# Kernel optimization log

Measured on AMD Instinct MI355X. Metric: run time of the kernel, lower is better.

## Reference

```python
import jax, jax.numpy as jnp
import numpy as np
from jax import lax

B, T, N = 512, 512, 64  # batch, max_seq_len, num_tags


def setup_inputs() -> dict:
    key = jax.random.key(0)
    k1, k2, k3, k4 = jax.random.split(key, 4)
    inputs = jax.random.normal(k1, (B, T, N), dtype=jnp.float32)
    transition_params = jax.random.normal(k2, (N, N), dtype=jnp.float32)
    tag_indices = jax.random.randint(k3, (B, T), 0, N, dtype=jnp.int32)
    sequence_lengths = jax.random.randint(k4, (B,), 0, T, dtype=jnp.int32)
    return {
        "inputs": inputs,
        "transition_params": transition_params,
        "tag_indices": tag_indices,
        "sequence_lengths": sequence_lengths,
    }


def _crf_log_norm(inputs, transition_params, sequence_lengths):
    # inputs: [B, T, N]
    first = inputs[:, 0, :]                       # alpha after first token, [B, N]
    rest = jnp.transpose(inputs[:, 1:, :], (1, 0, 2))  # [T-1, B, N]

    def step(alpha, emit):
        # alpha: [B, N] -> broadcast-add transitions [N, N], logsumexp over prev tag
        new = emit + jax.nn.logsumexp(alpha[:, :, None] + transition_params[None], axis=1)
        return new, new

    _, alphas = lax.scan(step, first, rest)       # [T-1, B, N]
    all_alphas = jnp.concatenate([first[None], alphas], axis=0)  # [T, B, N]
    all_alphas = jnp.transpose(all_alphas, (1, 0, 2))            # [B, T, N]
    last_index = jnp.maximum(0, sequence_lengths - 1)            # [B]
    alpha_last = jnp.take_along_axis(all_alphas, last_index[:, None, None], axis=1)[:, 0, :]
    return jax.nn.logsumexp(alpha_last, axis=1)   # [B]


def _crf_sequence_score(inputs, tag_indices, sequence_lengths, transition_params):
    mask = (jnp.arange(T)[None, :] < sequence_lengths[:, None]).astype(inputs.dtype)  # [B, T]
    # unary: gather emission score of the gold tag at each position
    unary = jnp.take_along_axis(inputs, tag_indices[:, :, None], axis=2)[:, :, 0]      # [B, T]
    unary_scores = jnp.sum(unary * mask, axis=1)
    # binary: transition scores between consecutive gold tags
    binary = transition_params[tag_indices[:, :-1], tag_indices[:, 1:]]                # [B, T-1]
    binary_scores = jnp.sum(binary * mask[:, 1:], axis=1)
    return unary_scores + binary_scores


def reference(inputs, transition_params, tag_indices, sequence_lengths):
    tag_indices = tag_indices.astype(jnp.int32)
    sequence_lengths = sequence_lengths.astype(jnp.int32)
    sequence_scores = _crf_sequence_score(inputs, tag_indices, sequence_lengths, transition_params)
    log_norm = _crf_log_norm(inputs, transition_params, sequence_lengths)
    log_likelihood = sequence_scores - log_norm   # [B]
    return (log_likelihood, transition_params)
```

## Files before the change

kernel.cpp:

```cpp
#include <hip/hip_runtime.h>

#define BB 512
#define TT 512
#define NN 64

__device__ __forceinline__ float readlane_f(float v, int lane) {
    return __int_as_float(__builtin_amdgcn_readlane(__float_as_int(v), lane));
}


#define S2(x) #x
#define S1(x) S2(x)

#define FMAC_DPP(ACC, QB, EV, R) \
    asm("v_fmac_f32_dpp %0, %1, %2 row_ror:" S1(R) " row_mask:0xf bank_mask:0xf" \
        : "+v"(ACC) : "v"(QB), "v"(EV));
#define MUL_DPP(DST, QB, EV, R) \
    asm("v_mul_f32_dpp %0, %1, %2 row_ror:" S1(R) " row_mask:0xf bank_mask:0xf" \
        : "=v"(DST) : "v"(QB), "v"(EV));

#define BLK_FIRST(QB, C0, C1, C2, C3) \
    a0 = QB * C0.x; \
    MUL_DPP(a1, QB, C0.y, 1)  MUL_DPP(a2, QB, C0.z, 2)  MUL_DPP(a3, QB, C0.w, 3) \
    FMAC_DPP(a0, QB, C1.x, 4)  FMAC_DPP(a1, QB, C1.y, 5) \
    FMAC_DPP(a2, QB, C1.z, 6)  FMAC_DPP(a3, QB, C1.w, 7) \
    FMAC_DPP(a0, QB, C2.x, 8)  FMAC_DPP(a1, QB, C2.y, 9) \
    FMAC_DPP(a2, QB, C2.z, 10) FMAC_DPP(a3, QB, C2.w, 11) \
    FMAC_DPP(a0, QB, C3.x, 12) FMAC_DPP(a1, QB, C3.y, 13) \
    FMAC_DPP(a2, QB, C3.z, 14) FMAC_DPP(a3, QB, C3.w, 15)

#define BLK(QB, C0, C1, C2, C3) \
    a0 = fmaf(QB, C0.x, a0); \
    FMAC_DPP(a1, QB, C0.y, 1)  FMAC_DPP(a2, QB, C0.z, 2)  FMAC_DPP(a3, QB, C0.w, 3) \
    FMAC_DPP(a0, QB, C1.x, 4)  FMAC_DPP(a1, QB, C1.y, 5) \
    FMAC_DPP(a2, QB, C1.z, 6)  FMAC_DPP(a3, QB, C1.w, 7) \
    FMAC_DPP(a0, QB, C2.x, 8)  FMAC_DPP(a1, QB, C2.y, 9) \
    FMAC_DPP(a2, QB, C2.z, 10) FMAC_DPP(a3, QB, C2.w, 11) \
    FMAC_DPP(a0, QB, C3.x, 12) FMAC_DPP(a1, QB, C3.y, 13) \
    FMAC_DPP(a2, QB, C3.z, 14) FMAC_DPP(a3, QB, C3.w, 15)

#define STEP(tc_, EM, RESC) { \
    asm("s_nop 1" : "+v"(q));    \
    const int qi = __float_as_int(q); \
    const float q1 = __int_as_float(__builtin_amdgcn_ds_bpermute(a16, qi)); \
    const float q2 = __int_as_float(__builtin_amdgcn_ds_bpermute(a32, qi)); \
    const float q3 = __int_as_float(__builtin_amdgcn_ds_bpermute(a48, qi)); \
    float a0, a1, a2, a3; \
    BLK_FIRST(q, D00, D01, D02, D03) \
    BLK(q1, D10, D11, D12, D13) \
    BLK(q2, D20, D21, D22, D23) \
    BLK(q3, D30, D31, D32, D33) \
    const float s = (a0 + a1) + (a2 + a3); \
    float qn; \
    if (RESC) { \
        const int sb = __float_as_int(readlane_f(s, 0)); \
        const int kb = ((sb >> 23) & 255) - 127; \
        const float sf = __int_as_float((127 - kb) << 23);   \
        qn = (s * (EM)) * sf; \
        if ((tc_) <= last) kcum += kb; \
    } else { \
        qn = s * (EM); \
    } \
    q = ((tc_) <= last) ? qn : q; \
}

__global__ __launch_bounds__(64, 1) void crf_kernel(
    const float* __restrict__ inputs,
    const float* __restrict__ trans,
    const int*   __restrict__ tags,
    const int*   __restrict__ lens,
    float*       __restrict__ out)
{
    const int b = blockIdx.x;
    const int j = threadIdx.x;

    if (b < 64) out[BB + b * 64 + j] = trans[b * 64 + j];

    const int L    = lens[b];
    const int last = (L - 1) > 0 ? (L - 1) : 0;

    const float* inb  = inputs + (size_t)b * TT * NN;
    const int*   tagb = tags + (size_t)b * TT;

    float sc = 0.f;
    #pragma unroll
    for (int k = 0; k < 8; ++k) {
        const int t  = k * 64 + j;
        const int tg = tagb[t];
        if (t < L) sc += inb[t * NN + tg];
        if (t + 1 < L) sc += trans[tg * NN + tagb[t + 1]];
    }
    #pragma unroll
    for (int x = 32; x >= 1; x >>= 1) sc += __shfl_xor(sc, x, 64);

    const int pr  = __builtin_amdgcn_update_dpp(0, j, 0x121 ,
                                                0xf, 0xf, false);
    const int r0p = __builtin_amdgcn_readlane(pr, 0);
    const int dhw = (r0p == 1) ? 1 : -1;

    float4 D00, D01, D02, D03, D10, D11, D12, D13;
    float4 D20, D21, D22, D23, D30, D31, D32, D33;
#define LDD(DST, B, R) { \
    const int rr = (j + dhw * (R)) & 15; \
    const int ii = (((j & 48) | rr) + 16 * (B)) & 63; \
    DST = __expf(trans[ii * NN + j]); }
#define LDD4(V, B, R0) LDD(V.x, B, R0) LDD(V.y, B, (R0)+1) \
                       LDD(V.z, B, (R0)+2) LDD(V.w, B, (R0)+3)
    LDD4(D00, 0, 0) LDD4(D01, 0, 4) LDD4(D02, 0, 8) LDD4(D03, 0, 12)
    LDD4(D10, 1, 0) LDD4(D11, 1, 4) LDD4(D12, 1, 8) LDD4(D13, 1, 12)
    LDD4(D20, 2, 0) LDD4(D21, 2, 4) LDD4(D22, 2, 8) LDD4(D23, 2, 12)
    LDD4(D30, 3, 0) LDD4(D31, 3, 4) LDD4(D32, 3, 8) LDD4(D33, 3, 12)
#undef LDD4
#undef LDD

    const int a16 = ((j + 16) & 63) * 4;
    const int a32 = ((j + 32) & 63) * 4;
    const int a48 = ((j + 48) & 63) * 4;

    const float alpha0 = inb[j];
    const float m0 = readlane_f(alpha0, 0);
    float q = __expf(alpha0 - m0);
    int kcum = 0;

    float4 fA0, fA1, fB0, fB1;

#define LD(vec, comp, tt) { const int tc_ = (tt) <= last ? (tt) : last; \
                            vec.comp = inb[tc_ * NN + j]; }
#define LOAD8(v0, v1, base) \
    LD(v0, x, (base) + 0) LD(v0, y, (base) + 1) LD(v0, z, (base) + 2) LD(v0, w, (base) + 3) \
    LD(v1, x, (base) + 4) LD(v1, y, (base) + 5) LD(v1, z, (base) + 6) LD(v1, w, (base) + 7)
#define EXP8(v0, v1) \
    v0.x = __expf(v0.x); v0.y = __expf(v0.y); v0.z = __expf(v0.z); v0.w = __expf(v0.w); \
    v1.x = __expf(v1.x); v1.y = __expf(v1.y); v1.z = __expf(v1.z); v1.w = __expf(v1.w);

    LOAD8(fA0, fA1, 1)
    EXP8(fA0, fA1)

    for (int t0 = 1; t0 <= last; t0 += 16) {
        LOAD8(fB0, fB1, t0 + 8)
        STEP(t0 + 0, fA0.x, 0) STEP(t0 + 1, fA0.y, 0)
        STEP(t0 + 2, fA0.z, 0) STEP(t0 + 3, fA0.w, 1)
        STEP(t0 + 4, fA1.x, 0) STEP(t0 + 5, fA1.y, 0)
        STEP(t0 + 6, fA1.z, 0) STEP(t0 + 7, fA1.w, 1)
        EXP8(fB0, fB1)
        LOAD8(fA0, fA1, t0 + 16)
        STEP(t0 + 8,  fB0.x, 0) STEP(t0 + 9,  fB0.y, 0)
        STEP(t0 + 10, fB0.z, 0) STEP(t0 + 11, fB0.w, 1)
        STEP(t0 + 12, fB1.x, 0) STEP(t0 + 13, fB1.y, 0)
        STEP(t0 + 14, fB1.z, 0) STEP(t0 + 15, fB1.w, 1)
        EXP8(fA0, fA1)
    }
#undef EXP8
#undef LOAD8
#undef LD

    float qs = q;
    #pragma unroll
    for (int x = 32; x >= 1; x >>= 1) qs += __shfl_xor(qs, x, 64);
    if (j == 0) {
        const double C = (double)m0 + (double)kcum * 0.6931471805599453;
        out[b] = sc - (float)((double)__logf(qs) + C);
    }
}

extern "C" void kernel_launch(void* const* d_in, const int* in_sizes, int n_in,
                              void* d_out, int out_size, void* d_ws, size_t ws_size,
                              hipStream_t stream) {
    const float* inputs = (const float*)d_in[0];
    const float* trans  = (const float*)d_in[1];
    const int*   tags   = (const int*)d_in[2];
    const int*   lens   = (const int*)d_in[3];
    float*       out    = (float*)d_out;

    crf_kernel<<<dim3(BB), dim3(64), 0, stream>>>(inputs, trans, tags, lens, out);
}
```

Measured before the change: 202.7 us.

## Stream exp-transition coefficients from LDS each step instead of holding in registers

The 64 precomputed exp(transition) values per lane are stored in shared memory in an XOR-swizzled layout, and each recurrence step re-reads them with ds_read_b128 into registers, issued after the step together with the three bpermutes. Hand-written asm with explicit lgkmcnt waits and sched barriers controls the ordering. The aim is to cut register pressure or free the scheduler, and to overlap the LDS reads with the cross-lane bpermute latency. In exchange, every one of the roughly 512 serial steps now issues 16 extra LDS loads and waits on all of them before its FMACs can run.

Result: slower. 226.2 us (+11.6%).

```diff
diff --git a/kernel.cpp b/kernel.cpp
--- a/kernel.cpp
+++ b/kernel.cpp
@@ -1,4 +1,5 @@
 #include <hip/hip_runtime.h>
+#include <stdint.h>
 
 #define BB 512
 #define TT 512
@@ -13,11 +14,17 @@
 #define S1(x) S2(x)
 
 #define FMAC_DPP(ACC, QB, EV, R) \
-    asm("v_fmac_f32_dpp %0, %1, %2 row_ror:" S1(R) " row_mask:0xf bank_mask:0xf" \
+    asm volatile("v_fmac_f32_dpp %0, %1, %2 row_ror:" S1(R) " row_mask:0xf bank_mask:0xf" \
         : "+v"(ACC) : "v"(QB), "v"(EV));
 #define MUL_DPP(DST, QB, EV, R) \
-    asm("v_mul_f32_dpp %0, %1, %2 row_ror:" S1(R) " row_mask:0xf bank_mask:0xf" \
+    asm volatile("v_mul_f32_dpp %0, %1, %2 row_ror:" S1(R) " row_mask:0xf bank_mask:0xf" \
         : "=v"(DST) : "v"(QB), "v"(EV));
+#define RD1(Cv, AD) \
+    asm volatile("ds_read_b128 %0, %1" : "=v"(Cv) : "v"(AD));
+#define BPERM(DST, AD, SRC) \
+    asm volatile("ds_bpermute_b32 %0, %1, %2" : "=v"(DST) : "v"(AD), "v"(SRC));
+#define WAITLG0 { asm volatile("s_waitcnt lgkmcnt(0)"); \
+                  __builtin_amdgcn_sched_barrier(0); }
 
 #define BLK_FIRST(QB, C0, C1, C2, C3) \
     a0 = QB * C0.x; \
@@ -39,17 +46,20 @@
     FMAC_DPP(a0, QB, C3.x, 12) FMAC_DPP(a1, QB, C3.y, 13) \
     FMAC_DPP(a2, QB, C3.z, 14) FMAC_DPP(a3, QB, C3.w, 15)
 
+#define REFILL \
+    BPERM(q1, a16, q) BPERM(q2, a32, q) BPERM(q3, a48, q) \
+    RD1(C00, ad0)  RD1(C01, ad1)  RD1(C02, ad2)  RD1(C03, ad3) \
+    RD1(C10, ad4)  RD1(C11, ad5)  RD1(C12, ad6)  RD1(C13, ad7) \
+    RD1(C20, ad8)  RD1(C21, ad9)  RD1(C22, ad10) RD1(C23, ad11) \
+    RD1(C30, ad12) RD1(C31, ad13) RD1(C32, ad14) RD1(C33, ad15)
+
 #define STEP(tc_, EM, RESC) { \
-    asm("s_nop 1" : "+v"(q));    \
-    const int qi = __float_as_int(q); \
-    const float q1 = __int_as_float(__builtin_amdgcn_ds_bpermute(a16, qi)); \
-    const float q2 = __int_as_float(__builtin_amdgcn_ds_bpermute(a32, qi)); \
-    const float q3 = __int_as_float(__builtin_amdgcn_ds_bpermute(a48, qi)); \
+    WAITLG0 \
     float a0, a1, a2, a3; \
-    BLK_FIRST(q, D00, D01, D02, D03) \
-    BLK(q1, D10, D11, D12, D13) \
-    BLK(q2, D20, D21, D22, D23) \
-    BLK(q3, D30, D31, D32, D33) \
+    BLK_FIRST(q,  C00, C01, C02, C03) \
+    BLK(q1, C10, C11, C12, C13) \
+    BLK(q2, C20, C21, C22, C23) \
+    BLK(q3, C30, C31, C32, C33) \
     const float s = (a0 + a1) + (a2 + a3); \
     float qn; \
     if (RESC) { \
@@ -62,6 +72,7 @@
         qn = s * (EM); \
     } \
     q = ((tc_) <= last) ? qn : q; \
+    REFILL \
 }
 
 __global__ __launch_bounds__(64, 1) void crf_kernel(
@@ -98,21 +109,30 @@
     const int r0p = __builtin_amdgcn_readlane(pr, 0);
     const int dhw = (r0p == 1) ? 1 : -1;
 
-    float4 D00, D01, D02, D03, D10, D11, D12, D13;
-    float4 D20, D21, D22, D23, D30, D31, D32, D33;
-#define LDD(DST, B, R) { \
-    const int rr = (j + dhw * (R)) & 15; \
-    const int ii = (((j & 48) | rr) + 16 * (B)) & 63; \
-    DST = __expf(trans[ii * NN + j]); }
-#define LDD4(V, B, R0) LDD(V.x, B, R0) LDD(V.y, B, (R0)+1) \
-                       LDD(V.z, B, (R0)+2) LDD(V.w, B, (R0)+3)
-    LDD4(D00, 0, 0) LDD4(D01, 0, 4) LDD4(D02, 0, 8) LDD4(D03, 0, 12)
-    LDD4(D10, 1, 0) LDD4(D11, 1, 4) LDD4(D12, 1, 8) LDD4(D13, 1, 12)
-    LDD4(D20, 2, 0) LDD4(D21, 2, 4) LDD4(D22, 2, 8) LDD4(D23, 2, 12)
-    LDD4(D30, 3, 0) LDD4(D31, 3, 4) LDD4(D32, 3, 8) LDD4(D33, 3, 12)
-#undef LDD4
-#undef LDD
-
+    __shared__ __align__(16) float4 DL4[NN * 16];
+    const int jx = j & 15;
+    #pragma unroll
+    for (int bb = 0; bb < 4; ++bb) {
+        #pragma unroll
+        for (int k = 0; k < 4; ++k) {
+            float4 v;
+            #define DV(c) { const int r = 4 * k + (c); \
+                const int ii = (((j & 48) | ((j + dhw * r) & 15)) + 16 * bb) & 63; \
+                ((float*)&v)[c] = __expf(trans[ii * NN + j]); }
+            DV(0) DV(1) DV(2) DV(3)
+            #undef DV
+            DL4[j * 16 + ((4 * bb + k) ^ jx)] = v;
+        }
+    }
+    asm volatile("s_waitcnt lgkmcnt(0)" ::: "memory");
+    __builtin_amdgcn_sched_barrier(0);
+
+    #define ADR(S) ((uint32_t)(uintptr_t)(&DL4[j * 16 + ((S) ^ jx)]))
+    const uint32_t ad0  = ADR(0),  ad1  = ADR(1),  ad2  = ADR(2),  ad3  = ADR(3);
+    const uint32_t ad4  = ADR(4),  ad5  = ADR(5),  ad6  = ADR(6),  ad7  = ADR(7);
+    const uint32_t ad8  = ADR(8),  ad9  = ADR(9),  ad10 = ADR(10), ad11 = ADR(11);
+    const uint32_t ad12 = ADR(12), ad13 = ADR(13), ad14 = ADR(14), ad15 = ADR(15);
+    #undef ADR
     const int a16 = ((j + 16) & 63) * 4;
     const int a32 = ((j + 32) & 63) * 4;
     const int a48 = ((j + 48) & 63) * 4;
@@ -121,6 +141,12 @@
     const float m0 = readlane_f(alpha0, 0);
     float q = __expf(alpha0 - m0);
     int kcum = 0;
+
+    float4 C00, C01, C02, C03, C10, C11, C12, C13;
+    float4 C20, C21, C22, C23, C30, C31, C32, C33;
+    float q1, q2, q3;
+
+    REFILL
 
     float4 fA0, fA1, fB0, fB1;
 
```
